# Optimization experiments

Hardware: AMD Instinct MI355X
Metric: run time of the kernel (lower is better)

Reference implementation:

```python
import jax, jax.numpy as jnp
import numpy as np

N = 50000        # nodes
E = 800000       # edges
F_IN = 16        # num_features
F_EDGE = 8       # num_edge_features
H = 4            # heads
C = 32           # hidden_dim (per-head out channels)
D = H * C        # 128, node state width
NUM_CLASSES = 5
NEG_SLOPE = 0.2  # PyG GATConv default leaky_relu slope


def setup_inputs() -> dict:
    key = jax.random.key(0)
    ks = jax.random.split(key, 30)
    def w(k, shape):
        return jax.random.normal(k, shape, dtype=jnp.float32) * 0.05
    return {
        "x": jax.random.normal(ks[0], (N, F_IN), dtype=jnp.float32),
        "edge_index": jax.random.randint(ks[1], (2, E), 0, N),
        "edge_attr": jax.random.normal(ks[2], (E, F_EDGE), dtype=jnp.float32),
        # edge_encoder: Linear(F_EDGE->C), ReLU, Linear(C->H)
        "ee_w1": w(ks[3], (C, F_EDGE)), "ee_b1": jnp.zeros((C,), jnp.float32),
        "ee_w2": w(ks[4], (H, C)),      "ee_b2": jnp.zeros((H,), jnp.float32),
        # input_proj: Linear(F_IN -> D)
        "proj_w": w(ks[5], (D, F_IN)), "proj_b": jnp.zeros((D,), jnp.float32),
        # conv1: GATConv(F_IN, C, heads=H, edge_dim=H, concat=True)
        "c1_lin": w(ks[6], (D, F_IN)),
        "c1_att_src": w(ks[7], (H, C)), "c1_att_dst": w(ks[8], (H, C)),
        "c1_lin_edge": w(ks[9], (D, H)), "c1_att_edge": w(ks[10], (H, C)),
        "c1_bias": jnp.zeros((D,), jnp.float32),
        # conv2: GATConv(D, C, heads=H, edge_dim=H, concat=True)
        "c2_lin": w(ks[11], (D, D)),
        "c2_att_src": w(ks[12], (H, C)), "c2_att_dst": w(ks[13], (H, C)),
        "c2_lin_edge": w(ks[14], (D, H)), "c2_att_edge": w(ks[15], (H, C)),
        "c2_bias": jnp.zeros((D,), jnp.float32),
        # layer norms
        "n1_g": jnp.ones((D,), jnp.float32), "n1_b": jnp.zeros((D,), jnp.float32),
        "n2_g": jnp.ones((D,), jnp.float32), "n2_b": jnp.zeros((D,), jnp.float32),
        # jk_proj: Linear(3D -> D)
        "jk_w": w(ks[16], (D, 3 * D)), "jk_b": jnp.zeros((D,), jnp.float32),
        # classifier: Linear(D -> NUM_CLASSES)
        "cls_w": w(ks[17], (NUM_CLASSES, D)), "cls_b": jnp.zeros((NUM_CLASSES,), jnp.float32),
    }


def _layer_norm(h, g, b, eps=1e-5):
    mu = jnp.mean(h, axis=-1, keepdims=True)
    var = jnp.var(h, axis=-1, keepdims=True)
    return (h - mu) * jax.lax.rsqrt(var + eps) * g + b


def _gat_conv(x, src, dst, e_attr, lin_w, att_src, att_dst, lin_edge_w, att_edge, bias):
    """PyG GATConv (v1) with edge features, concat=True, eval mode (no dropout)."""
    n = x.shape[0]
    xs = (x @ lin_w.T).reshape(n, H, C)                      # [N,H,C]
    a_src = jnp.einsum('nhc,hc->nh', xs, att_src)            # [N,H]
    a_dst = jnp.einsum('nhc,hc->nh', xs, att_dst)            # [N,H]
    ee = (e_attr @ lin_edge_w.T).reshape(-1, H, C)           # [E,H,C]
    a_edge = jnp.einsum('ehc,hc->eh', ee, att_edge)          # [E,H]
    alpha = jax.nn.leaky_relu(a_src[src] + a_dst[dst] + a_edge, NEG_SLOPE)
    # segment softmax over destination neighborhoods
    amax = jax.ops.segment_max(alpha, dst, num_segments=n)
    ex = jnp.exp(alpha - amax[dst])
    denom = jax.ops.segment_sum(ex, dst, num_segments=n)
    alpha = ex / (denom[dst] + 1e-16)                        # [E,H]
    msg = xs[src] * alpha[:, :, None]                        # [E,H,C]
    out = jax.ops.segment_sum(msg, dst, num_segments=n)      # [N,H,C]
    return out.reshape(n, H * C) + bias


def reference(x, edge_index, edge_attr,
              ee_w1, ee_b1, ee_w2, ee_b2,
              proj_w, proj_b,
              c1_lin, c1_att_src, c1_att_dst, c1_lin_edge, c1_att_edge, c1_bias,
              c2_lin, c2_att_src, c2_att_dst, c2_lin_edge, c2_att_edge, c2_bias,
              n1_g, n1_b, n2_g, n2_b,
              jk_w, jk_b, cls_w, cls_b):
    src, dst = edge_index[0], edge_index[1]
    # edge encoder
    e = jax.nn.relu(edge_attr @ ee_w1.T + ee_b1) @ ee_w2.T + ee_b2   # [E,H]
    h0 = x @ proj_w.T + proj_b                                        # [N,D]
    h1 = _gat_conv(x, src, dst, e, c1_lin, c1_att_src, c1_att_dst,
                   c1_lin_edge, c1_att_edge, c1_bias)
    h1 = _layer_norm(jax.nn.elu(h1) + h0, n1_g, n1_b)
    h2 = _gat_conv(h1, src, dst, e, c2_lin, c2_att_src, c2_att_dst,
                   c2_lin_edge, c2_att_edge, c2_bias)
    h2 = _layer_norm(jax.nn.elu(h2) + h1, n2_g, n2_b)
    h = jnp.concatenate([h0, h1, h2], axis=-1) @ jk_w.T + jk_b
    out = h @ cls_w.T + cls_b
    return jax.nn.log_softmax(out, axis=1)
```

## Files before the change

kernel.cpp:

```cpp
#include <hip/hip_runtime.h>
#include <cstdint>

#define NN 50000
#define NE 800000
#define DPX 6250
#define SLICES 391

using short8  = __attribute__((ext_vector_type(8))) short;
using float4v = __attribute__((ext_vector_type(4))) float;

__device__ __forceinline__ ushort f2bf(float f) {
    uint u = __float_as_uint(f);
    uint r = (u + 0x7fffu + ((u >> 16) & 1u)) >> 16;
    return (ushort)r;
}
__device__ __forceinline__ float bf2f(uint u) {
    return __uint_as_float(u << 16);
}

__global__ __launch_bounds__(256) void k_prep2(const float* __restrict__ le1, const float* __restrict__ ae1,
                                               const float* __restrict__ le2, const float* __restrict__ ae2,
                                               const float* __restrict__ jkw, const float* __restrict__ jkb,
                                               const float* __restrict__ clw, const float* __restrict__ clb,
                                               const float* __restrict__ projw, const float* __restrict__ c1lin,
                                               const float* __restrict__ c2lin,
                                               const float* __restrict__ asrc1, const float* __restrict__ adst1,
                                               float* __restrict__ M, float* __restrict__ CW,
                                               float* __restrict__ cbp,
                                               ushort* __restrict__ w01b, ushort* __restrict__ c2b,
                                               float* __restrict__ Vmat, int* __restrict__ deg)
{
    int idx = blockIdx.x * 256 + threadIdx.x;
    if (idx < NN) deg[idx] = 0;
    if (idx < 32) {
        const float* le = (idx < 16) ? le1 : le2;
        const float* ae = (idx < 16) ? ae1 : ae2;
        int hk = idx & 15, h = hk >> 2, k = hk & 3;
        float s = 0.f;
        for (int c = 0; c < 32; ++c)
            s += le[(h * 32 + c) * 4 + k] * ae[h * 32 + c];
        M[idx] = s;
    } else if (idx < 1952) {
        int o = idx - 32;
        int r = o / 384, c = o - r * 384;
        float s = 0.f;
        for (int k = 0; k < 128; ++k)
            s += clw[r * 128 + k] * jkw[(size_t)k * 384 + c];
        CW[o] = s;
    } else if (idx < 1957) {
        int r = idx - 1952;
        float s = clb[r];
        for (int k = 0; k < 128; ++k)
            s += clw[r * 128 + k] * jkb[k];
        cbp[r] = s;
    } else if (idx >= 2048 && idx < 10240) {
        int o = idx - 2048;
        int r = o >> 5, c = o & 31;
        float v = 0.f;
        if (c < 16) v = (r < 128) ? projw[r * 16 + c] : c1lin[(r - 128) * 16 + c];
        w01b[o] = f2bf(v);
    } else if (idx >= 10240 && idx < 26624) {
        int o = idx - 10240;
        c2b[o] = f2bf(c2lin[o]);
    } else if (idx >= 26624 && idx < 26752) {
        int o = idx - 26624;
        const float* att = (o < 64) ? asrc1 : adst1;
        int oo = o & 63, h = oo >> 4, k = oo & 15;
        float s = 0.f;
        for (int c = 0; c < 32; ++c)
            s += c1lin[(h * 32 + c) * 16 + k] * att[h * 32 + c];
        Vmat[o] = s;
    }
}

__global__ __launch_bounds__(256) void k_att1(const float* __restrict__ x,
                                              const float* __restrict__ V,
                                              float* __restrict__ as_o,
                                              float* __restrict__ ad_o)
{
    __shared__ float sV[128];
    int t = threadIdx.x;
    if (t < 128) sV[t] = V[t];
    __syncthreads();
    int n = blockIdx.x * 256 + t;
    if (n >= NN) return;
    const float4* xr = (const float4*)(x + (size_t)n * 16);
    float4 x0 = xr[0], x1 = xr[1], x2 = xr[2], x3 = xr[3];
    float xv[16] = {x0.x,x0.y,x0.z,x0.w, x1.x,x1.y,x1.z,x1.w,
                    x2.x,x2.y,x2.z,x2.w, x3.x,x3.y,x3.z,x3.w};
    float s[4], d[4];
    #pragma unroll
    for (int h = 0; h < 4; ++h) {
        float ss = 0.f, dd = 0.f;
        #pragma unroll
        for (int k = 0; k < 16; ++k) {
            ss += xv[k] * sV[h * 16 + k];
            dd += xv[k] * sV[64 + h * 16 + k];
        }
        s[h] = ss; d[h] = dd;
    }
    *(float4*)(as_o + (size_t)n * 4) = make_float4(s[0], s[1], s[2], s[3]);
    *(float4*)(ad_o + (size_t)n * 4) = make_float4(d[0], d[1], d[2], d[3]);
}

__global__ __launch_bounds__(256) void k_edge_mlp(const float* __restrict__ ea,
                                                  const float* __restrict__ w1,
                                                  const float* __restrict__ b1,
                                                  const float* __restrict__ w2,
                                                  const float* __restrict__ b2,
                                                  const int* __restrict__ ei,
                                                  const float* __restrict__ Mm,
                                                  const float* __restrict__ as1,
                                                  const float* __restrict__ ad1,
                                                  ushort* __restrict__ exb,
                                                  ushort* __restrict__ ae2)
{
    __shared__ float sw1[256], sb1[32], sw2[128], sb2[4], sM[32];
    int t = threadIdx.x;
    sw1[t] = w1[t];
    if (t < 128) sw2[t] = w2[t];
    if (t < 32)  { sb1[t] = b1[t]; sM[t] = Mm[t]; }
    if (t < 4)   sb2[t] = b2[t];
    __syncthreads();
    int e = blockIdx.x * 256 + t;
    if (e >= NE) return;
    int src = ei[e], dst = ei[NE + e];
    float4 s4 = *(const float4*)(as1 + (size_t)src * 4);
    float4 d4 = *(const float4*)(ad1 + (size_t)dst * 4);
    float4 x0 = *(const float4*)(ea + (size_t)e * 8);
    float4 x1 = *(const float4*)(ea + (size_t)e * 8 + 4);
    float o0 = sb2[0], o1 = sb2[1], o2 = sb2[2], o3 = sb2[3];
    #pragma unroll
    for (int j = 0; j < 32; ++j) {
        const float* w = sw1 + j * 8;
        float s = sb1[j] + w[0]*x0.x + w[1]*x0.y + w[2]*x0.z + w[3]*x0.w
                         + w[4]*x1.x + w[5]*x1.y + w[6]*x1.z + w[7]*x1.w;
        s = fmaxf(s, 0.f);
        o0 += sw2[0*32+j] * s; o1 += sw2[1*32+j] * s;
        o2 += sw2[2*32+j] * s; o3 += sw2[3*32+j] * s;
    }
    float sa[4] = {s4.x, s4.y, s4.z, s4.w};
    float da[4] = {d4.x, d4.y, d4.z, d4.w};
    ushort exq[4], a2q[4];
    #pragma unroll
    for (int h = 0; h < 4; ++h) {
        float ae1 = sM[h*4+0]*o0 + sM[h*4+1]*o1 + sM[h*4+2]*o2 + sM[h*4+3]*o3;
        float al = sa[h] + da[h] + ae1;
        al = al > 0.f ? al : 0.2f * al;
        exq[h] = f2bf(__expf(al));
        a2q[h] = f2bf(sM[16+h*4+0]*o0 + sM[16+h*4+1]*o1 + sM[16+h*4+2]*o2 + sM[16+h*4+3]*o3);
    }
    *(uint2*)(exb + (size_t)e * 4) =
        make_uint2((uint)exq[0] | ((uint)exq[1] << 16), (uint)exq[2] | ((uint)exq[3] << 16));
    *(uint2*)(ae2 + (size_t)e * 4) =
        make_uint2((uint)a2q[0] | ((uint)a2q[1] << 16), (uint)a2q[2] | ((uint)a2q[3] << 16));
}

__global__ __launch_bounds__(256) void k_hist8(const int* __restrict__ ei, int* __restrict__ deg)
{
    int grp = blockIdx.x & 7;
    int base = (blockIdx.x >> 3) * 2048 + threadIdx.x;
    #pragma unroll
    for (int k = 0; k < 8; ++k) {
        int e = base + k * 256;
        if (e < NE) {
            int dst = ei[NE + e];
            if (dst / DPX == grp) atomicAdd(&deg[dst], 1);
        }
    }
}

__global__ __launch_bounds__(256) void k_scan_blk(const int* __restrict__ deg,
                                                  int* __restrict__ loc,
                                                  int* __restrict__ bsum)
{
    __shared__ int tmp[256];
    int t = threadIdx.x;
    int i = blockIdx.x * 256 + t;
    int v = (i < NN) ? deg[i] : 0;
    tmp[t] = v;
    __syncthreads();
    #pragma unroll
    for (int o = 1; o < 256; o <<= 1) {
        int add = (t >= o) ? tmp[t - o] : 0;
        __syncthreads();
        tmp[t] += add;
        __syncthreads();
    }
    if (i < NN) loc[i] = tmp[t] - v;
    if (t == 255) bsum[blockIdx.x] = tmp[255];
}

__global__ __launch_bounds__(256) void k_scan_top(const int* __restrict__ bsum,
                                                  int* __restrict__ bcarry,
                                                  int* __restrict__ total_out, int nb)
{
    __shared__ int tmp[256];
    int t = threadIdx.x;
    int v = (t < nb) ? bsum[t] : 0;
    tmp[t] = v;
    __syncthreads();
    #pragma unroll
    for (int o = 1; o < 256; o <<= 1) {
        int add = (t >= o) ? tmp[t - o] : 0;
        __syncthreads();
        tmp[t] += add;
        __syncthreads();
    }
    if (t < nb) bcarry[t] = tmp[t] - v;
    if (t == 255) *total_out = tmp[255];
}

__global__ __launch_bounds__(256) void k_scan_add(const int* __restrict__ loc,
                                                  const int* __restrict__ bcarry,
                                                  int* __restrict__ off,
                                                  int* __restrict__ cur)
{
    int i = blockIdx.x * 256 + threadIdx.x;
    if (i < NN) {
        int o = loc[i] + bcarry[blockIdx.x];
        off[i] = o;
        cur[i] = o;
    }
}

__global__ __launch_bounds__(256) void k_scatter8(const int* __restrict__ ei,
                                                  const ushort* __restrict__ exb,
                                                  int* __restrict__ cursor,
                                                  int4* __restrict__ csr4)
{
    int grp = blockIdx.x & 7;
    int base = (blockIdx.x >> 3) * 2048 + threadIdx.x;
    #pragma unroll
    for (int k = 0; k < 8; ++k) {
        int e = base + k * 256;
        if (e < NE) {
            int dst = ei[NE + e];
            if (dst / DPX == grp) {
                int src = ei[e];
                uint2 ex = *(const uint2*)(exb + (size_t)e * 4);
                int p = atomicAdd(&cursor[dst], 1);
                csr4[p] = make_int4((src << 16) | dst, e, (int)ex.x, (int)ex.y);
            }
        }
    }
}

__global__ __launch_bounds__(256) void k_gemm1(const float* __restrict__ x,
                                               const ushort* __restrict__ w01,
                                               const float* __restrict__ pbias,
                                               ushort* __restrict__ hcatb,
                                               ushort* __restrict__ xs, int M)
{
    int t = threadIdx.x;
    int wv = t >> 6, lane = t & 63;
    int quad = lane >> 4, r16 = lane & 15;
    int m0 = blockIdx.x * 128 + wv * 32;
    int ar0 = m0 + r16;      if (ar0 >= M) ar0 = M - 1;
    int ar1 = m0 + 16 + r16; if (ar1 >= M) ar1 = M - 1;
    short8 a0 = (short8){0,0,0,0,0,0,0,0}, a1 = a0;
    if (quad < 2) {
        const float* p0 = x + (size_t)ar0 * 16 + quad * 8;
        const float* p1 = x + (size_t)ar1 * 16 + quad * 8;
        float4 u0 = *(const float4*)p0, u1 = *(const float4*)(p0 + 4);
        float4 v0 = *(const float4*)p1, v1 = *(const float4*)(p1 + 4);
        a0[0]=(short)f2bf(u0.x); a0[1]=(short)f2bf(u0.y); a0[2]=(short)f2bf(u0.z); a0[3]=(short)f2bf(u0.w);
        a0[4]=(short)f2bf(u1.x); a0[5]=(short)f2bf(u1.y); a0[6]=(short)f2bf(u1.z); a0[7]=(short)f2bf(u1.w);
        a1[0]=(short)f2bf(v0.x); a1[1]=(short)f2bf(v0.y); a1[2]=(short)f2bf(v0.z); a1[3]=(short)f2bf(v0.w);
        a1[4]=(short)f2bf(v1.x); a1[5]=(short)f2bf(v1.y); a1[6]=(short)f2bf(v1.z); a1[7]=(short)f2bf(v1.w);
    }
    float4v acc[2][16];
    #pragma unroll
    for (int i = 0; i < 2; ++i)
        #pragma unroll
        for (int j = 0; j < 16; ++j) acc[i][j] = (float4v){0.f, 0.f, 0.f, 0.f};
    #pragma unroll
    for (int nt = 0; nt < 16; ++nt) {
        short8 b = *(const short8*)(w01 + (size_t)(nt * 16 + r16) * 32 + quad * 8);
        acc[0][nt] = __builtin_amdgcn_mfma_f32_16x16x32_bf16(a0, b, acc[0][nt], 0, 0, 0);
        acc[1][nt] = __builtin_amdgcn_mfma_f32_16x16x32_bf16(a1, b, acc[1][nt], 0, 0, 0);
    }
    #pragma unroll
    for (int rt = 0; rt < 2; ++rt) {
        #pragma unroll
        for (int nt = 0; nt < 16; ++nt) {
            int col = (nt & 7) * 16 + r16;
            float bv = (nt < 8) ? pbias[col] : 0.f;
            #pragma unroll
            for (int r = 0; r < 4; ++r) {
                int row = m0 + rt * 16 + quad * 4 + r;
                if (row < M) {
                    float v = acc[rt][nt][r] + bv;
                    if (nt < 8) hcatb[(size_t)row * 384 + col] = f2bf(v);
                    else        xs[(size_t)row * 128 + col] = f2bf(v);
                }
            }
        }
    }
}

__global__ __launch_bounds__(256) void k_gemm2(const ushort* __restrict__ A,
                                               const ushort* __restrict__ W,
                                               const float* __restrict__ atts,
                                               const float* __restrict__ attd,
                                               ushort* __restrict__ xs,
                                               float* __restrict__ as_o,
                                               float* __restrict__ ad_o, int M)
{
    __shared__ float sAs[128], sAd[128];
    int t = threadIdx.x;
    if (t < 128) { sAs[t] = atts[t]; sAd[t] = attd[t]; }
    __syncthreads();
    int wv = t >> 6, lane = t & 63;
    int quad = lane >> 4, r16 = lane & 15;
    int m0 = blockIdx.x * 128 + wv * 32;
    float4v acc[2][8];
    #pragma unroll
    for (int i = 0; i < 2; ++i)
        #pragma unroll
        for (int j = 0; j < 8; ++j) acc[i][j] = (float4v){0.f, 0.f, 0.f, 0.f};
    int ar0 = m0 + r16;      if (ar0 >= M) ar0 = M - 1;
    int ar1 = m0 + 16 + r16; if (ar1 >= M) ar1 = M - 1;
    const ushort* a0p = A + (size_t)ar0 * 384 + quad * 8;
    const ushort* a1p = A + (size_t)ar1 * 384 + quad * 8;
    const ushort* wp  = W + (size_t)r16 * 128 + quad * 8;
    #pragma unroll
    for (int k0 = 0; k0 < 128; k0 += 32) {
        short8 a0 = *(const short8*)(a0p + k0);
        short8 a1 = *(const short8*)(a1p + k0);
        #pragma unroll
        for (int nt = 0; nt < 8; ++nt) {
            short8 b = *(const short8*)(wp + (size_t)(nt * 16) * 128 + k0);
            acc[0][nt] = __builtin_amdgcn_mfma_f32_16x16x32_bf16(a0, b, acc[0][nt], 0, 0, 0);
            acc[1][nt] = __builtin_amdgcn_mfma_f32_16x16x32_bf16(a1, b, acc[1][nt], 0, 0, 0);
        }
    }
    #pragma unroll
    for (int rt = 0; rt < 2; ++rt) {
        #pragma unroll
        for (int nt = 0; nt < 8; ++nt) {
            int col = nt * 16 + r16;
            #pragma unroll
            for (int r = 0; r < 4; ++r) {
                int row = m0 + rt * 16 + quad * 4 + r;
                if (row < M)
                    xs[(size_t)row * 128 + col] = f2bf(acc[rt][nt][r]);
            }
        }
        #pragma unroll
        for (int r = 0; r < 4; ++r) {
            int row = m0 + rt * 16 + quad * 4 + r;
            float sh[4], dh[4];
            #pragma unroll
            for (int h = 0; h < 4; ++h) {
                int cA = h * 32 + r16, cB = cA + 16;
                sh[h] = acc[rt][2*h][r] * sAs[cA] + acc[rt][2*h+1][r] * sAs[cB];
                dh[h] = acc[rt][2*h][r] * sAd[cA] + acc[rt][2*h+1][r] * sAd[cB];
            }
            #pragma unroll
            for (int o = 1; o < 16; o <<= 1) {
                #pragma unroll
                for (int h = 0; h < 4; ++h) {
                    sh[h] += __shfl_xor(sh[h], o, 64);
                    dh[h] += __shfl_xor(dh[h], o, 64);
                }
            }
            if (r16 == 0 && row < M) {
                *(float4*)(as_o + (size_t)row * 4) = make_float4(sh[0], sh[1], sh[2], sh[3]);
                *(float4*)(ad_o + (size_t)row * 4) = make_float4(dh[0], dh[1], dh[2], dh[3]);
            }
        }
    }
}

__global__ __launch_bounds__(256) void k_soft2csr(int4* __restrict__ csr4,
                                                  const float* __restrict__ as_in,
                                                  const float* __restrict__ ad_in,
                                                  const ushort* __restrict__ ae2)
{
    int i = blockIdx.x * 256 + threadIdx.x;
    if (i >= NE) return;
    int4 en = csr4[i];
    uint sd = (uint)en.x;
    int src = (int)(sd >> 16), dst = (int)(sd & 0xffffu);
    float4 s4 = *(const float4*)(as_in + (size_t)src * 4);
    float4 d4 = *(const float4*)(ad_in + (size_t)dst * 4);
    uint2 aq = *(const uint2*)(ae2 + (size_t)en.y * 4);
    float av[4] = {bf2f(aq.x & 0xffffu), bf2f(aq.x >> 16), bf2f(aq.y & 0xffffu), bf2f(aq.y >> 16)};
    float sa[4] = {s4.x, s4.y, s4.z, s4.w};
    float da[4] = {d4.x, d4.y, d4.z, d4.w};
    ushort exq[4];
    #pragma unroll
    for (int h = 0; h < 4; ++h) {
        float al = sa[h] + da[h] + av[h];
        al = al > 0.f ? al : 0.2f * al;
        exq[h] = f2bf(__expf(al));
    }
    en.z = (int)((uint)exq[0] | ((uint)exq[1] << 16));
    en.w = (int)((uint)exq[2] | ((uint)exq[3] << 16));
    csr4[i] = en;
}

__global__ __launch_bounds__(256) void k_agg2(const int* __restrict__ off,
                                              const int4* __restrict__ csr4,
                                              const ushort* __restrict__ xs,
                                              const float* __restrict__ bias,
                                              const ushort* __restrict__ residb,
                                              const float* __restrict__ g,
                                              const float* __restrict__ bln,
                                              ushort* __restrict__ outb)
{
    int wave = threadIdx.x >> 6;
    int lane = threadIdx.x & 63;
    int n = blockIdx.x * 4 + wave;
    if (n >= NN) return;
    int i0 = off[n], i1 = off[n + 1];
    int c0 = lane * 2;
    int h = lane >> 4;
    int hsel = h >> 1, hsh = (h & 1) << 4;
    float a0 = 0.f, a1 = 0.f, den = 0.f;
    int i = i0;
    for (; i + 8 <= i1; i += 8) {
        int4 en[8];
        #pragma unroll
        for (int j = 0; j < 8; ++j) en[j] = csr4[i + j];
        uint p[8];
        #pragma unroll
        for (int j = 0; j < 8; ++j)
            p[j] = *(const uint*)(xs + (size_t)((uint)en[j].x >> 16) * 128 + c0);
        #pragma unroll
        for (int j = 0; j < 8; ++j) {
            uint exsel = (uint)(hsel ? en[j].w : en[j].z);
            float w = bf2f((exsel >> hsh) & 0xffffu);
            a0 = fmaf(bf2f(p[j] & 0xffffu), w, a0);
            a1 = fmaf(bf2f(p[j] >> 16), w, a1);
            den += w;
        }
    }
    for (; i + 4 <= i1; i += 4) {
        int4 en[4];
        #pragma unroll
        for (int j = 0; j < 4; ++j) en[j] = csr4[i + j];
        uint p[4];
        #pragma unroll
        for (int j = 0; j < 4; ++j)
            p[j] = *(const uint*)(xs + (size_t)((uint)en[j].x >> 16) * 128 + c0);
        #pragma unroll
        for (int j = 0; j < 4; ++j) {
            uint exsel = (uint)(hsel ? en[j].w : en[j].z);
            float w = bf2f((exsel >> hsh) & 0xffffu);
            a0 = fmaf(bf2f(p[j] & 0xffffu), w, a0);
            a1 = fmaf(bf2f(p[j] >> 16), w, a1);
            den += w;
        }
    }
    for (; i < i1; ++i) {
        int4 en = csr4[i];
        uint p0 = *(const uint*)(xs + (size_t)((uint)en.x >> 16) * 128 + c0);
        uint exsel = (uint)(hsel ? en.w : en.z);
        float w = bf2f((exsel >> hsh) & 0xffffu);
        a0 = fmaf(bf2f(p0 & 0xffffu), w, a0);
        a1 = fmaf(bf2f(p0 >> 16), w, a1);
        den += w;
    }
    float inv = 1.f / (den + 1e-16f);
    float v0 = a0 * inv + bias[c0];
    float v1 = a1 * inv + bias[c0 + 1];
    v0 = v0 > 0.f ? v0 : (__expf(v0) - 1.f);
    v1 = v1 > 0.f ? v1 : (__expf(v1) - 1.f);
    uint rp = *(const uint*)(residb + (size_t)n * 384 + c0);
    float r0 = v0 + bf2f(rp & 0xffffu);
    float r1 = v1 + bf2f(rp >> 16);
    float ssum = r0 + r1, ssq = r0 * r0 + r1 * r1;
    #pragma unroll
    for (int o = 1; o < 64; o <<= 1) {
        ssum += __shfl_xor(ssum, o, 64);
        ssq  += __shfl_xor(ssq, o, 64);
    }
    float mu = ssum * (1.f / 128.f);
    float var = ssq * (1.f / 128.f) - mu * mu;
    float rs = rsqrtf(var + 1e-5f);
    float o0 = (r0 - mu) * rs * g[c0] + bln[c0];
    float o1 = (r1 - mu) * rs * g[c0 + 1] + bln[c0 + 1];
    uint pk = (uint)f2bf(o0) | ((uint)f2bf(o1) << 16);
    *(uint*)(outb + (size_t)n * 384 + c0) = pk;
}

__global__ __launch_bounds__(256) void k_cls(const ushort* __restrict__ hcatb,
                                             const float* __restrict__ CW,
                                             const float* __restrict__ cbp,
                                             float* __restrict__ out)
{
    __shared__ float sCW[1920], scb[5];
    int t = threadIdx.x;
    for (int i = t; i < 1920; i += 256) sCW[i] = CW[i];
    if (t < 5) scb[t] = cbp[t];
    __syncthreads();
    int n = blockIdx.x * 256 + t;
    if (n >= NN) return;
    float acc[5] = {scb[0], scb[1], scb[2], scb[3], scb[4]};
    const uint2* hr = (const uint2*)(hcatb + (size_t)n * 384);
    #pragma unroll 4
    for (int q = 0; q < 96; ++q) {
        uint2 p = hr[q];
        float v0 = bf2f(p.x & 0xffffu), v1 = bf2f(p.x >> 16);
        float v2 = bf2f(p.y & 0xffffu), v3 = bf2f(p.y >> 16);
        #pragma unroll
        for (int o = 0; o < 5; ++o) {
            const float* w = sCW + o * 384 + q * 4;
            acc[o] += v0*w[0] + v1*w[1] + v2*w[2] + v3*w[3];
        }
    }
    float m = acc[0];
    #pragma unroll
    for (int o = 1; o < 5; ++o) m = fmaxf(m, acc[o]);
    float sum = 0.f;
    #pragma unroll
    for (int o = 0; o < 5; ++o) sum += __expf(acc[o] - m);
    float lse = __logf(sum) + m;
    float* op = out + (size_t)n * 5;
    #pragma unroll
    for (int o = 0; o < 5; ++o) op[o] = acc[o] - lse;
}

extern "C" void kernel_launch(void* const* d_in, const int* in_sizes, int n_in,
                              void* d_out, int out_size, void* d_ws, size_t ws_size,
                              hipStream_t stream)
{
    (void)in_sizes; (void)n_in; (void)out_size; (void)ws_size;
    const float* x        = (const float*)d_in[0];
    const int*   ei       = (const int*)d_in[1];
    const float* eattr    = (const float*)d_in[2];
    const float* ee_w1    = (const float*)d_in[3];
    const float* ee_b1    = (const float*)d_in[4];
    const float* ee_w2    = (const float*)d_in[5];
    const float* ee_b2    = (const float*)d_in[6];
    const float* proj_w   = (const float*)d_in[7];
    const float* proj_b   = (const float*)d_in[8];
    const float* c1_lin   = (const float*)d_in[9];
    const float* c1_asrc  = (const float*)d_in[10];
    const float* c1_adst  = (const float*)d_in[11];
    const float* c1_ledge = (const float*)d_in[12];
    const float* c1_aedge = (const float*)d_in[13];
    const float* c1_bias  = (const float*)d_in[14];
    const float* c2_lin   = (const float*)d_in[15];
    const float* c2_asrc  = (const float*)d_in[16];
    const float* c2_adst  = (const float*)d_in[17];
    const float* c2_ledge = (const float*)d_in[18];
    const float* c2_aedge = (const float*)d_in[19];
    const float* c2_bias  = (const float*)d_in[20];
    const float* n1_g     = (const float*)d_in[21];
    const float* n1_b     = (const float*)d_in[22];
    const float* n2_g     = (const float*)d_in[23];
    const float* n2_b     = (const float*)d_in[24];
    const float* jk_w     = (const float*)d_in[25];
    const float* jk_b     = (const float*)d_in[26];
    const float* cls_w    = (const float*)d_in[27];
    const float* cls_b    = (const float*)d_in[28];
    float* out = (float*)d_out;
    float* ws  = (float*)d_ws;

    const size_t oM   = 0;
    const size_t oCW  = 64;
    const size_t oCB  = 1984;
    const size_t oV   = 2048;
    const size_t oEX  = 2176;
    const size_t oAE2 = oEX + (size_t)NE * 2;
    const size_t oHB  = oAE2 + (size_t)NE * 2;
    const size_t oXS  = oHB + (size_t)NN * 192;
    const size_t oWB  = oXS + (size_t)NN * 64;
    const size_t oAS  = oWB + 12288;
    const size_t oAD  = oAS + (size_t)NN * 4;
    const size_t oI   = oAD + (size_t)NN * 4;

    float*  Mmat  = ws + oM;
    float*  CW    = ws + oCW;
    float*  cbp   = ws + oCB;
    float*  Vmat  = ws + oV;
    ushort* exb   = (ushort*)(ws + oEX);
    ushort* ae2b  = (ushort*)(ws + oAE2);
    ushort* hcatb = (ushort*)(ws + oHB);
    ushort* xs    = (ushort*)(ws + oXS);
    ushort* w01b  = (ushort*)(ws + oWB);
    ushort* c2b   = w01b + 8192;
    float*  as_b  = ws + oAS;
    float*  ad_b  = ws + oAD;
    int*    ip    = (int*)(ws + oI);
    int*    deg   = ip;
    int*    loc   = ip + NN;
    int*    off   = ip + 2 * NN;
    int*    cur   = ip + 3 * NN + 16;
    int*    bsum  = ip + 4 * NN + 16;
    int*    bcar  = ip + 4 * NN + 272;
    int4*   csr4  = (int4*)(ip + 4 * NN + 544);

    const int EB  = (NE + 255) / 256;
    const int NB  = (NN + 255) / 256;
    const int GB  = (NN + 127) / 128;
    const int WB2 = (NN + 3) / 4;
    const int PB  = SLICES * 8;

    k_prep2<<<NB, 256, 0, stream>>>(c1_ledge, c1_aedge, c2_ledge, c2_aedge,
                                    jk_w, jk_b, cls_w, cls_b,
                                    proj_w, c1_lin, c2_lin, c1_asrc, c1_adst,
                                    Mmat, CW, cbp, w01b, c2b, Vmat, deg);
    k_att1<<<NB, 256, 0, stream>>>(x, Vmat, as_b, ad_b);
    k_edge_mlp<<<EB, 256, 0, stream>>>(eattr, ee_w1, ee_b1, ee_w2, ee_b2, ei,
                                       Mmat, as_b, ad_b, exb, ae2b);
    k_hist8<<<PB, 256, 0, stream>>>(ei, deg);
    k_scan_blk<<<NB, 256, 0, stream>>>(deg, loc, bsum);
    k_scan_top<<<1, 256, 0, stream>>>(bsum, bcar, off + NN, NB);
    k_scan_add<<<NB, 256, 0, stream>>>(loc, bcar, off, cur);
    k_scatter8<<<PB, 256, 0, stream>>>(ei, exb, cur, csr4);

    k_gemm1<<<GB, 256, 0, stream>>>(x, w01b, proj_b, hcatb, xs, NN);

    k_agg2<<<WB2, 256, 0, stream>>>(off, csr4, xs, c1_bias, hcatb,
                                    n1_g, n1_b, hcatb + 128);

    k_gemm2<<<GB, 256, 0, stream>>>(hcatb + 128, c2b, c2_asrc, c2_adst,
                                    xs, as_b, ad_b, NN);
    k_soft2csr<<<EB, 256, 0, stream>>>(csr4, as_b, ad_b, ae2b);
    k_agg2<<<WB2, 256, 0, stream>>>(off, csr4, xs, c2_bias, hcatb + 128,
                                    n2_g, n2_b, hcatb + 256);

    k_cls<<<NB, 256, 0, stream>>>(hcatb, CW, cbp, out);
}
```

Measured before the change: 393.4 us.

## Store gathered node features as FP8 and pre-permute edge attention into CSR order

The projected node features that the aggregation kernels gather per edge are now stored as FP8 (e4m3) instead of bf16. This halves the bytes of the random gather traffic in both aggregation passes, and the values are converted back with the packed fp8-to-f32 instruction. Separately, the second-layer edge attention terms are written in CSR order during the scatter, so the softmax kernel reads them sequentially instead of through the original edge index. The softmax kernel also now writes only the half of the CSR entry that changes. FP8 storage reduces precision of the message values and may affect accuracy.

```diff
diff --git a/kernel.cpp b/kernel.cpp
--- a/kernel.cpp
+++ b/kernel.cpp
@@ -8,6 +8,8 @@
 
 using short8  = __attribute__((ext_vector_type(8))) short;
 using float4v = __attribute__((ext_vector_type(4))) float;
+using floatx2 = __attribute__((ext_vector_type(2))) float;
+typedef unsigned char uchar;
 
 __device__ __forceinline__ ushort f2bf(float f) {
     uint u = __float_as_uint(f);
@@ -16,6 +18,9 @@
 }
 __device__ __forceinline__ float bf2f(uint u) {
     return __uint_as_float(u << 16);
+}
+__device__ __forceinline__ uchar f2fp8(float v) {
+    return (uchar)((uint)__builtin_amdgcn_cvt_pk_fp8_f32(v, v, 0, false) & 0xffu);
 }
 
 __global__ __launch_bounds__(256) void k_prep2(const float* __restrict__ le1, const float* __restrict__ ae1,
@@ -226,8 +231,10 @@
 
 __global__ __launch_bounds__(256) void k_scatter8(const int* __restrict__ ei,
                                                   const ushort* __restrict__ exb,
+                                                  const ushort* __restrict__ ae2b,
                                                   int* __restrict__ cursor,
-                                                  int4* __restrict__ csr4)
+                                                  int4* __restrict__ csr4,
+                                                  uint2* __restrict__ ae2csr)
 {
     int grp = blockIdx.x & 7;
     int base = (blockIdx.x >> 3) * 2048 + threadIdx.x;
@@ -239,8 +246,10 @@
             if (dst / DPX == grp) {
                 int src = ei[e];
                 uint2 ex = *(const uint2*)(exb + (size_t)e * 4);
+                uint2 ae = *(const uint2*)(ae2b + (size_t)e * 4);
                 int p = atomicAdd(&cursor[dst], 1);
                 csr4[p] = make_int4((src << 16) | dst, e, (int)ex.x, (int)ex.y);
+                ae2csr[p] = ae;
             }
         }
     }
@@ -250,7 +259,7 @@
                                                const ushort* __restrict__ w01,
                                                const float* __restrict__ pbias,
                                                ushort* __restrict__ hcatb,
-                                               ushort* __restrict__ xs, int M)
+                                               uchar* __restrict__ xs8, int M)
 {
     int t = threadIdx.x;
     int wv = t >> 6, lane = t & 63;
@@ -292,7 +301,7 @@
                 if (row < M) {
                     float v = acc[rt][nt][r] + bv;
                     if (nt < 8) hcatb[(size_t)row * 384 + col] = f2bf(v);
-                    else        xs[(size_t)row * 128 + col] = f2bf(v);
+                    else        xs8[(size_t)row * 128 + col] = f2fp8(v);
                 }
             }
         }
@@ -303,7 +312,7 @@
                                                const ushort* __restrict__ W,
                                                const float* __restrict__ atts,
                                                const float* __restrict__ attd,
-                                               ushort* __restrict__ xs,
+                                               uchar* __restrict__ xs8,
                                                float* __restrict__ as_o,
                                                float* __restrict__ ad_o, int M)
 {
@@ -344,7 +353,7 @@
             for (int r = 0; r < 4; ++r) {
                 int row = m0 + rt * 16 + quad * 4 + r;
                 if (row < M)
-                    xs[(size_t)row * 128 + col] = f2bf(acc[rt][nt][r]);
+                    xs8[(size_t)row * 128 + col] = f2fp8(acc[rt][nt][r]);
             }
         }
         #pragma unroll
@@ -374,18 +383,17 @@
 }
 
 __global__ __launch_bounds__(256) void k_soft2csr(int4* __restrict__ csr4,
+                                                  const uint2* __restrict__ ae2csr,
                                                   const float* __restrict__ as_in,
-                                                  const float* __restrict__ ad_in,
-                                                  const ushort* __restrict__ ae2)
+                                                  const float* __restrict__ ad_in)
 {
     int i = blockIdx.x * 256 + threadIdx.x;
     if (i >= NE) return;
-    int4 en = csr4[i];
-    uint sd = (uint)en.x;
+    uint sd = (uint)csr4[i].x;
     int src = (int)(sd >> 16), dst = (int)(sd & 0xffffu);
     float4 s4 = *(const float4*)(as_in + (size_t)src * 4);
     float4 d4 = *(const float4*)(ad_in + (size_t)dst * 4);
-    uint2 aq = *(const uint2*)(ae2 + (size_t)en.y * 4);
+    uint2 aq = ae2csr[i];
     float av[4] = {bf2f(aq.x & 0xffffu), bf2f(aq.x >> 16), bf2f(aq.y & 0xffffu), bf2f(aq.y >> 16)};
     float sa[4] = {s4.x, s4.y, s4.z, s4.w};
     float da[4] = {d4.x, d4.y, d4.z, d4.w};
@@ -396,14 +404,13 @@
         al = al > 0.f ? al : 0.2f * al;
         exq[h] = f2bf(__expf(al));
     }
-    en.z = (int)((uint)exq[0] | ((uint)exq[1] << 16));
-    en.w = (int)((uint)exq[2] | ((uint)exq[3] << 16));
-    csr4[i] = en;
+    ((uint2*)&csr4[i])[1] =
+        make_uint2((uint)exq[0] | ((uint)exq[1] << 16), (uint)exq[2] | ((uint)exq[3] << 16));
 }
 
 __global__ __launch_bounds__(256) void k_agg2(const int* __restrict__ off,
                                               const int4* __restrict__ csr4,
-                                              const ushort* __restrict__ xs,
+                                              const uchar* __restrict__ xs8,
                                               const float* __restrict__ bias,
                                               const ushort* __restrict__ residb,
                                               const float* __restrict__ g,
@@ -424,16 +431,17 @@
         int4 en[8];
         #pragma unroll
         for (int j = 0; j < 8; ++j) en[j] = csr4[i + j];
-        uint p[8];
+        ushort p[8];
         #pragma unroll
         for (int j = 0; j < 8; ++j)
-            p[j] = *(const uint*)(xs + (size_t)((uint)en[j].x >> 16) * 128 + c0);
+            p[j] = *(const ushort*)(xs8 + (size_t)((uint)en[j].x >> 16) * 128 + c0);
         #pragma unroll
         for (int j = 0; j < 8; ++j) {
             uint exsel = (uint)(hsel ? en[j].w : en[j].z);
             float w = bf2f((exsel >> hsh) & 0xffffu);
-            a0 = fmaf(bf2f(p[j] & 0xffffu), w, a0);
-            a1 = fmaf(bf2f(p[j] >> 16), w, a1);
+            floatx2 v = __builtin_amdgcn_cvt_pk_f32_fp8((int)(uint)p[j], false);
+            a0 = fmaf(v.x, w, a0);
+            a1 = fmaf(v.y, w, a1);
             den += w;
         }
     }
@@ -441,26 +449,28 @@
         int4 en[4];
         #pragma unroll
         for (int j = 0; j < 4; ++j) en[j] = csr4[i + j];
-        uint p[4];
+        ushort p[4];
         #pragma unroll
         for (int j = 0; j < 4; ++j)
-            p[j] = *(const uint*)(xs + (size_t)((uint)en[j].x >> 16) * 128 + c0);
+            p[j] = *(const ushort*)(xs8 + (size_t)((uint)en[j].x >> 16) * 128 + c0);
         #pragma unroll
         for (int j = 0; j < 4; ++j) {
             uint exsel = (uint)(hsel ? en[j].w : en[j].z);
             float w = bf2f((exsel >> hsh) & 0xffffu);
-            a0 = fmaf(bf2f(p[j] & 0xffffu), w, a0);
-            a1 = fmaf(bf2f(p[j] >> 16), w, a1);
+            floatx2 v = __builtin_amdgcn_cvt_pk_f32_fp8((int)(uint)p[j], false);
+            a0 = fmaf(v.x, w, a0);
+            a1 = fmaf(v.y, w, a1);
             den += w;
         }
     }
     for (; i < i1; ++i) {
         int4 en = csr4[i];
-        uint p0 = *(const uint*)(xs + (size_t)((uint)en.x >> 16) * 128 + c0);
+        ushort p0 = *(const ushort*)(xs8 + (size_t)((uint)en.x >> 16) * 128 + c0);
         uint exsel = (uint)(hsel ? en.w : en.z);
         float w = bf2f((exsel >> hsh) & 0xffffu);
-        a0 = fmaf(bf2f(p0 & 0xffffu), w, a0);
-        a1 = fmaf(bf2f(p0 >> 16), w, a1);
+        floatx2 v = __builtin_amdgcn_cvt_pk_f32_fp8((int)(uint)p0, false);
+        a0 = fmaf(v.x, w, a0);
+        a1 = fmaf(v.y, w, a1);
         den += w;
     }
     float inv = 1.f / (den + 1e-16f);
@@ -568,7 +578,7 @@
     const size_t oAE2 = oEX + (size_t)NE * 2;
     const size_t oHB  = oAE2 + (size_t)NE * 2;
     const size_t oXS  = oHB + (size_t)NN * 192;
-    const size_t oWB  = oXS + (size_t)NN * 64;
+    const size_t oWB  = oXS + (size_t)NN * 32;
     const size_t oAS  = oWB + 12288;
     const size_t oAD  = oAS + (size_t)NN * 4;
     const size_t oI   = oAD + (size_t)NN * 4;
@@ -580,19 +590,20 @@
     ushort* exb   = (ushort*)(ws + oEX);
     ushort* ae2b  = (ushort*)(ws + oAE2);
     ushort* hcatb = (ushort*)(ws + oHB);
-    ushort* xs    = (ushort*)(ws + oXS);
+    uchar*  xs8   = (uchar*)(ws + oXS);
     ushort* w01b  = (ushort*)(ws + oWB);
     ushort* c2b   = w01b + 8192;
     float*  as_b  = ws + oAS;
     float*  ad_b  = ws + oAD;
     int*    ip    = (int*)(ws + oI);
-    int*    deg   = ip;
-    int*    loc   = ip + NN;
-    int*    off   = ip + 2 * NN;
-    int*    cur   = ip + 3 * NN + 16;
-    int*    bsum  = ip + 4 * NN + 16;
-    int*    bcar  = ip + 4 * NN + 272;
-    int4*   csr4  = (int4*)(ip + 4 * NN + 544);
+    int*    deg    = ip;
+    int*    loc    = ip + NN;
+    int*    off    = ip + 2 * NN;
+    int*    cur    = ip + 3 * NN + 16;
+    int*    bsum   = ip + 4 * NN + 16;
+    int*    bcar   = ip + 4 * NN + 272;
+    int4*   csr4   = (int4*)(ip + 4 * NN + 544);
+    uint2*  ae2csr = (uint2*)(ip + 4 * NN + 544 + 4 * (size_t)NE);
 
     const int EB  = (NE + 255) / 256;
     const int NB  = (NN + 255) / 256;
@@ -611,17 +622,17 @@
     k_scan_blk<<<NB, 256, 0, stream>>>(deg, loc, bsum);
     k_scan_top<<<1, 256, 0, stream>>>(bsum, bcar, off + NN, NB);
     k_scan_add<<<NB, 256, 0, stream>>>(loc, bcar, off, cur);
-    k_scatter8<<<PB, 256, 0, stream>>>(ei, exb, cur, csr4);
-
-    k_gemm1<<<GB, 256, 0, stream>>>(x, w01b, proj_b, hcatb, xs, NN);
-
-    k_agg2<<<WB2, 256, 0, stream>>>(off, csr4, xs, c1_bias, hcatb,
+    k_scatter8<<<PB, 256, 0, stream>>>(ei, exb, ae2b, cur, csr4, ae2csr);
+
+    k_gemm1<<<GB, 256, 0, stream>>>(x, w01b, proj_b, hcatb, xs8, NN);
+
+    k_agg2<<<WB2, 256, 0, stream>>>(off, csr4, xs8, c1_bias, hcatb,
                                     n1_g, n1_b, hcatb + 128);
 
     k_gemm2<<<GB, 256, 0, stream>>>(hcatb + 128, c2b, c2_asrc, c2_adst,
-                                    xs, as_b, ad_b, NN);
-    k_soft2csr<<<EB, 256, 0, stream>>>(csr4, as_b, ad_b, ae2b);
-    k_agg2<<<WB2, 256, 0, stream>>>(off, csr4, xs, c2_bias, hcatb + 128,
+                                    xs8, as_b, ad_b, NN);
+    k_soft2csr<<<EB, 256, 0, stream>>>(csr4, ae2csr, as_b, ad_b);
+    k_agg2<<<WB2, 256, 0, stream>>>(off, csr4, xs8, c2_bias, hcatb + 128,
                                     n2_g, n2_b, hcatb + 256);
 
     k_cls<<<NB, 256, 0, stream>>>(hcatb, CW, cbp, out);
```

New measurement: 393.5 us. Within noise of the previous version (+0.0%).

## Store node features as head-major fp8 and split aggregation per head

Applied to the files above, without the earlier changes.

Node features xs are now stored in fp8 in a head-major layout [head][node][32], so each gather fetches 32 bytes per head instead of 256-byte bf16 rows. The per-edge layer-2 edge attention terms are packed as fp8 directly into the CSR entries, which removes a separate indexed load in k_soft2csr. The fused aggregation kernel is split into k_aggH, which handles one head per block group across half of the nodes, and k_epi, which does normalization, ELU, residual and LayerNorm. This trades extra intermediate traffic and fp8 precision loss on activations for smaller gather footprints with better cache locality.

```diff
diff --git a/kernel.cpp b/kernel.cpp
--- a/kernel.cpp
+++ b/kernel.cpp
@@ -8,6 +8,8 @@
 
 using short8  = __attribute__((ext_vector_type(8))) short;
 using float4v = __attribute__((ext_vector_type(4))) float;
+using floatx2 = __attribute__((ext_vector_type(2))) float;
+typedef unsigned char uchar;
 
 __device__ __forceinline__ ushort f2bf(float f) {
     uint u = __float_as_uint(f);
@@ -16,6 +18,13 @@
 }
 __device__ __forceinline__ float bf2f(uint u) {
     return __uint_as_float(u << 16);
+}
+__device__ __forceinline__ uchar f2fp8(float v) {
+    return (uchar)((uint)__builtin_amdgcn_cvt_pk_fp8_f32(v, v, 0, false) & 0xffu);
+}
+__device__ __forceinline__ float fp8f(uint b) {
+    floatx2 v = __builtin_amdgcn_cvt_pk_f32_fp8((int)b, false);
+    return v.x;
 }
 
 __global__ __launch_bounds__(256) void k_prep2(const float* __restrict__ le1, const float* __restrict__ ae1,
@@ -113,7 +122,7 @@
                                                   const float* __restrict__ as1,
                                                   const float* __restrict__ ad1,
                                                   ushort* __restrict__ exb,
-                                                  ushort* __restrict__ ae2)
+                                                  uint* __restrict__ aeq)
 {
     __shared__ float sw1[256], sb1[32], sw2[128], sb2[4], sM[32];
     int t = threadIdx.x;
@@ -141,19 +150,21 @@
     }
     float sa[4] = {s4.x, s4.y, s4.z, s4.w};
     float da[4] = {d4.x, d4.y, d4.z, d4.w};
-    ushort exq[4], a2q[4];
+    ushort exq[4];
+    float a2[4];
     #pragma unroll
     for (int h = 0; h < 4; ++h) {
         float ae1 = sM[h*4+0]*o0 + sM[h*4+1]*o1 + sM[h*4+2]*o2 + sM[h*4+3]*o3;
         float al = sa[h] + da[h] + ae1;
         al = al > 0.f ? al : 0.2f * al;
         exq[h] = f2bf(__expf(al));
-        a2q[h] = f2bf(sM[16+h*4+0]*o0 + sM[16+h*4+1]*o1 + sM[16+h*4+2]*o2 + sM[16+h*4+3]*o3);
+        a2[h] = sM[16+h*4+0]*o0 + sM[16+h*4+1]*o1 + sM[16+h*4+2]*o2 + sM[16+h*4+3]*o3;
     }
     *(uint2*)(exb + (size_t)e * 4) =
         make_uint2((uint)exq[0] | ((uint)exq[1] << 16), (uint)exq[2] | ((uint)exq[3] << 16));
-    *(uint2*)(ae2 + (size_t)e * 4) =
-        make_uint2((uint)a2q[0] | ((uint)a2q[1] << 16), (uint)a2q[2] | ((uint)a2q[3] << 16));
+    uint q = (uint)__builtin_amdgcn_cvt_pk_fp8_f32(a2[0], a2[1], 0, false);
+    q = (uint)__builtin_amdgcn_cvt_pk_fp8_f32(a2[2], a2[3], (int)q, true);
+    aeq[e] = q;
 }
 
 __global__ __launch_bounds__(256) void k_hist8(const int* __restrict__ ei, int* __restrict__ deg)
@@ -226,6 +237,7 @@
 
 __global__ __launch_bounds__(256) void k_scatter8(const int* __restrict__ ei,
                                                   const ushort* __restrict__ exb,
+                                                  const uint* __restrict__ aeq,
                                                   int* __restrict__ cursor,
                                                   int4* __restrict__ csr4)
 {
@@ -239,8 +251,9 @@
             if (dst / DPX == grp) {
                 int src = ei[e];
                 uint2 ex = *(const uint2*)(exb + (size_t)e * 4);
+                uint q = aeq[e];
                 int p = atomicAdd(&cursor[dst], 1);
-                csr4[p] = make_int4((src << 16) | dst, e, (int)ex.x, (int)ex.y);
+                csr4[p] = make_int4((src << 16) | dst, (int)ex.x, (int)ex.y, (int)q);
             }
         }
     }
@@ -250,7 +263,7 @@
                                                const ushort* __restrict__ w01,
                                                const float* __restrict__ pbias,
                                                ushort* __restrict__ hcatb,
-                                               ushort* __restrict__ xs, int M)
+                                               uchar* __restrict__ xs8h, int M)
 {
     int t = threadIdx.x;
     int wv = t >> 6, lane = t & 63;
@@ -292,7 +305,7 @@
                 if (row < M) {
                     float v = acc[rt][nt][r] + bv;
                     if (nt < 8) hcatb[(size_t)row * 384 + col] = f2bf(v);
-                    else        xs[(size_t)row * 128 + col] = f2bf(v);
+                    else        xs8h[((size_t)(col >> 5) * NN + row) * 32 + (col & 31)] = f2fp8(v);
                 }
             }
         }
@@ -303,7 +316,7 @@
                                                const ushort* __restrict__ W,
                                                const float* __restrict__ atts,
                                                const float* __restrict__ attd,
-                                               ushort* __restrict__ xs,
+                                               uchar* __restrict__ xs8h,
                                                float* __restrict__ as_o,
                                                float* __restrict__ ad_o, int M)
 {
@@ -344,7 +357,7 @@
             for (int r = 0; r < 4; ++r) {
                 int row = m0 + rt * 16 + quad * 4 + r;
                 if (row < M)
-                    xs[(size_t)row * 128 + col] = f2bf(acc[rt][nt][r]);
+                    xs8h[((size_t)(col >> 5) * NN + row) * 32 + (col & 31)] = f2fp8(acc[rt][nt][r]);
             }
         }
         #pragma unroll
@@ -375,8 +388,7 @@
 
 __global__ __launch_bounds__(256) void k_soft2csr(int4* __restrict__ csr4,
                                                   const float* __restrict__ as_in,
-                                                  const float* __restrict__ ad_in,
-                                                  const ushort* __restrict__ ae2)
+                                                  const float* __restrict__ ad_in)
 {
     int i = blockIdx.x * 256 + threadIdx.x;
     if (i >= NE) return;
@@ -385,8 +397,9 @@
     int src = (int)(sd >> 16), dst = (int)(sd & 0xffffu);
     float4 s4 = *(const float4*)(as_in + (size_t)src * 4);
     float4 d4 = *(const float4*)(ad_in + (size_t)dst * 4);
-    uint2 aq = *(const uint2*)(ae2 + (size_t)en.y * 4);
-    float av[4] = {bf2f(aq.x & 0xffffu), bf2f(aq.x >> 16), bf2f(aq.y & 0xffffu), bf2f(aq.y >> 16)};
+    floatx2 a01 = __builtin_amdgcn_cvt_pk_f32_fp8(en.w, false);
+    floatx2 a23 = __builtin_amdgcn_cvt_pk_f32_fp8(en.w, true);
+    float av[4] = {a01.x, a01.y, a23.x, a23.y};
     float sa[4] = {s4.x, s4.y, s4.z, s4.w};
     float da[4] = {d4.x, d4.y, d4.z, d4.w};
     ushort exq[4];
@@ -396,94 +409,94 @@
         al = al > 0.f ? al : 0.2f * al;
         exq[h] = f2bf(__expf(al));
     }
-    en.z = (int)((uint)exq[0] | ((uint)exq[1] << 16));
-    en.w = (int)((uint)exq[2] | ((uint)exq[3] << 16));
+    en.y = (int)((uint)exq[0] | ((uint)exq[1] << 16));
+    en.z = (int)((uint)exq[2] | ((uint)exq[3] << 16));
     csr4[i] = en;
 }
 
-__global__ __launch_bounds__(256) void k_agg2(const int* __restrict__ off,
+__global__ __launch_bounds__(256) void k_aggH(const int* __restrict__ off,
                                               const int4* __restrict__ csr4,
-                                              const ushort* __restrict__ xs,
-                                              const float* __restrict__ bias,
-                                              const ushort* __restrict__ residb,
-                                              const float* __restrict__ g,
-                                              const float* __restrict__ bln,
-                                              ushort* __restrict__ outb)
-{
-    int wave = threadIdx.x >> 6;
-    int lane = threadIdx.x & 63;
-    int n = blockIdx.x * 4 + wave;
+                                              const uchar* __restrict__ xs8h,
+                                              ushort* __restrict__ aggH,
+                                              float* __restrict__ denH)
+{
+    int g = blockIdx.x & 7;
+    int head = g >> 1;
+    int bi = blockIdx.x >> 3;
+    int wave = threadIdx.x >> 6, lane = threadIdx.x & 63;
+    int n = (g & 1) * (NN / 2) + bi * 4 + wave;
     if (n >= NN) return;
     int i0 = off[n], i1 = off[n + 1];
-    int c0 = lane * 2;
-    int h = lane >> 4;
-    int hsel = h >> 1, hsh = (h & 1) << 4;
-    float a0 = 0.f, a1 = 0.f, den = 0.f;
-    int i = i0;
-    for (; i + 8 <= i1; i += 8) {
-        int4 en[8];
-        #pragma unroll
-        for (int j = 0; j < 8; ++j) en[j] = csr4[i + j];
-        uint p[8];
-        #pragma unroll
-        for (int j = 0; j < 8; ++j)
-            p[j] = *(const uint*)(xs + (size_t)((uint)en[j].x >> 16) * 128 + c0);
-        #pragma unroll
-        for (int j = 0; j < 8; ++j) {
-            uint exsel = (uint)(hsel ? en[j].w : en[j].z);
-            float w = bf2f((exsel >> hsh) & 0xffffu);
-            a0 = fmaf(bf2f(p[j] & 0xffffu), w, a0);
-            a1 = fmaf(bf2f(p[j] >> 16), w, a1);
-            den += w;
-        }
-    }
-    for (; i + 4 <= i1; i += 4) {
-        int4 en[4];
-        #pragma unroll
-        for (int j = 0; j < 4; ++j) en[j] = csr4[i + j];
-        uint p[4];
-        #pragma unroll
-        for (int j = 0; j < 4; ++j)
-            p[j] = *(const uint*)(xs + (size_t)((uint)en[j].x >> 16) * 128 + c0);
-        #pragma unroll
-        for (int j = 0; j < 4; ++j) {
-            uint exsel = (uint)(hsel ? en[j].w : en[j].z);
-            float w = bf2f((exsel >> hsh) & 0xffffu);
-            a0 = fmaf(bf2f(p[j] & 0xffffu), w, a0);
-            a1 = fmaf(bf2f(p[j] >> 16), w, a1);
-            den += w;
-        }
-    }
-    for (; i < i1; ++i) {
-        int4 en = csr4[i];
-        uint p0 = *(const uint*)(xs + (size_t)((uint)en.x >> 16) * 128 + c0);
-        uint exsel = (uint)(hsel ? en.w : en.z);
-        float w = bf2f((exsel >> hsh) & 0xffffu);
-        a0 = fmaf(bf2f(p0 & 0xffffu), w, a0);
-        a1 = fmaf(bf2f(p0 >> 16), w, a1);
-        den += w;
-    }
-    float inv = 1.f / (den + 1e-16f);
-    float v0 = a0 * inv + bias[c0];
-    float v1 = a1 * inv + bias[c0 + 1];
-    v0 = v0 > 0.f ? v0 : (__expf(v0) - 1.f);
-    v1 = v1 > 0.f ? v1 : (__expf(v1) - 1.f);
-    uint rp = *(const uint*)(residb + (size_t)n * 384 + c0);
-    float r0 = v0 + bf2f(rp & 0xffffu);
-    float r1 = v1 + bf2f(rp >> 16);
-    float ssum = r0 + r1, ssq = r0 * r0 + r1 * r1;
-    #pragma unroll
-    for (int o = 1; o < 64; o <<= 1) {
-        ssum += __shfl_xor(ssum, o, 64);
-        ssq  += __shfl_xor(ssq, o, 64);
-    }
-    float mu = ssum * (1.f / 128.f);
-    float var = ssq * (1.f / 128.f) - mu * mu;
+    int j = lane >> 5, c = lane & 31;
+    int hsel = head >> 1, hsh = (head & 1) << 4;
+    const uchar* xt = xs8h + (size_t)head * NN * 32 + c;
+    float a = 0.f, den = 0.f;
+    int i = i0 + j;
+    for (; i + 6 < i1; i += 8) {
+        int4 e0 = csr4[i], e1 = csr4[i+2], e2 = csr4[i+4], e3 = csr4[i+6];
+        uint b0 = xt[(size_t)((uint)e0.x >> 16) * 32];
+        uint b1 = xt[(size_t)((uint)e1.x >> 16) * 32];
+        uint b2 = xt[(size_t)((uint)e2.x >> 16) * 32];
+        uint b3 = xt[(size_t)((uint)e3.x >> 16) * 32];
+        float w0 = bf2f(((uint)(hsel ? e0.z : e0.y) >> hsh) & 0xffffu);
+        float w1 = bf2f(((uint)(hsel ? e1.z : e1.y) >> hsh) & 0xffffu);
+        float w2 = bf2f(((uint)(hsel ? e2.z : e2.y) >> hsh) & 0xffffu);
+        float w3 = bf2f(((uint)(hsel ? e3.z : e3.y) >> hsh) & 0xffffu);
+        a = fmaf(fp8f(b0), w0, a); a = fmaf(fp8f(b1), w1, a);
+        a = fmaf(fp8f(b2), w2, a); a = fmaf(fp8f(b3), w3, a);
+        den += (w0 + w1) + (w2 + w3);
+    }
+    for (; i < i1; i += 2) {
+        int4 e0 = csr4[i];
+        uint b0 = xt[(size_t)((uint)e0.x >> 16) * 32];
+        float w0 = bf2f(((uint)(hsel ? e0.z : e0.y) >> hsh) & 0xffffu);
+        a = fmaf(fp8f(b0), w0, a);
+        den += w0;
+    }
+    a += __shfl_xor(a, 32, 64);
+    den += __shfl_xor(den, 32, 64);
+    if (lane < 32) aggH[((size_t)head * NN + n) * 32 + c] = f2bf(a);
+    if (lane == 0) denH[(size_t)head * NN + n] = den;
+}
+
+__global__ __launch_bounds__(256) void k_epi(const ushort* __restrict__ aggH,
+                                             const float* __restrict__ denH,
+                                             const float* __restrict__ bias,
+                                             const ushort* __restrict__ residb,
+                                             const float* __restrict__ g,
+                                             const float* __restrict__ bln,
+                                             ushort* __restrict__ outb)
+{
+    __shared__ float red[4][2];
+    int t = threadIdx.x;
+    int n = blockIdx.x * 2 + (t >> 7);
+    int c = t & 127;
+    float r = 0.f;
+    if (n < NN) {
+        int h = c >> 5, cc = c & 31;
+        float a = bf2f(aggH[((size_t)h * NN + n) * 32 + cc]);
+        float den = denH[(size_t)h * NN + n];
+        float v = a / (den + 1e-16f) + bias[c];
+        v = v > 0.f ? v : (__expf(v) - 1.f);
+        r = v + bf2f(residb[(size_t)n * 384 + c]);
+    }
+    float s = r, sq = r * r;
+    #pragma unroll
+    for (int o = 32; o > 0; o >>= 1) {
+        s  += __shfl_down(s, o, 64);
+        sq += __shfl_down(sq, o, 64);
+    }
+    int wave = t >> 6;
+    if ((t & 63) == 0) { red[wave][0] = s; red[wave][1] = sq; }
+    __syncthreads();
+    int base = (t >> 7) * 2;
+    float S  = red[base][0] + red[base + 1][0];
+    float SQ = red[base][1] + red[base + 1][1];
+    float mu = S * (1.f / 128.f);
+    float var = SQ * (1.f / 128.f) - mu * mu;
     float rs = rsqrtf(var + 1e-5f);
-    float o0 = (r0 - mu) * rs * g[c0] + bln[c0];
-    float o1 = (r1 - mu) * rs * g[c0 + 1] + bln[c0 + 1];
-    uint pk = (uint)f2bf(o0) | ((uint)f2bf(o1) << 16);
-    *(uint*)(outb + (size_t)n * 384 + c0) = pk;
+    if (n < NN)
+        outb[(size_t)n * 384 + c] = f2bf((r - mu) * rs * g[c] + bln[c]);
 }
 
 __global__ __launch_bounds__(256) void k_cls(const ushort* __restrict__ hcatb,
@@ -565,10 +578,12 @@
     const size_t oCB  = 1984;
     const size_t oV   = 2048;
     const size_t oEX  = 2176;
-    const size_t oAE2 = oEX + (size_t)NE * 2;
-    const size_t oHB  = oAE2 + (size_t)NE * 2;
+    const size_t oAQ  = oEX + (size_t)NE * 2;
+    const size_t oHB  = oAQ + (size_t)NE;
     const size_t oXS  = oHB + (size_t)NN * 192;
-    const size_t oWB  = oXS + (size_t)NN * 64;
+    const size_t oAG  = oXS + (size_t)NN * 32;
+    const size_t oDN  = oAG + (size_t)NN * 64;
+    const size_t oWB  = oDN + (size_t)NN * 4;
     const size_t oAS  = oWB + 12288;
     const size_t oAD  = oAS + (size_t)NN * 4;
     const size_t oI   = oAD + (size_t)NN * 4;
@@ -578,9 +593,11 @@
     float*  cbp   = ws + oCB;
     float*  Vmat  = ws + oV;
     ushort* exb   = (ushort*)(ws + oEX);
-    ushort* ae2b  = (ushort*)(ws + oAE2);
+    uint*   aeq   = (uint*)(ws + oAQ);
     ushort* hcatb = (ushort*)(ws + oHB);
-    ushort* xs    = (ushort*)(ws + oXS);
+    uchar*  xs8h  = (uchar*)(ws + oXS);
+    ushort* aggH  = (ushort*)(ws + oAG);
+    float*  denH  = ws + oDN;
     ushort* w01b  = (ushort*)(ws + oWB);
     ushort* c2b   = w01b + 8192;
     float*  as_b  = ws + oAS;
@@ -597,8 +614,9 @@
     const int EB  = (NE + 255) / 256;
     const int NB  = (NN + 255) / 256;
     const int GB  = (NN + 127) / 128;
-    const int WB2 = (NN + 3) / 4;
     const int PB  = SLICES * 8;
+    const int AB  = (NN / 2 / 4) * 8;
+    const int PEB = NN / 2;
 
     k_prep2<<<NB, 256, 0, stream>>>(c1_ledge, c1_aedge, c2_ledge, c2_aedge,
                                     jk_w, jk_b, cls_w, cls_b,
@@ -606,23 +624,23 @@
                                     Mmat, CW, cbp, w01b, c2b, Vmat, deg);
     k_att1<<<NB, 256, 0, stream>>>(x, Vmat, as_b, ad_b);
     k_edge_mlp<<<EB, 256, 0, stream>>>(eattr, ee_w1, ee_b1, ee_w2, ee_b2, ei,
-                                       Mmat, as_b, ad_b, exb, ae2b);
+                                       Mmat, as_b, ad_b, exb, aeq);
     k_hist8<<<PB, 256, 0, stream>>>(ei, deg);
     k_scan_blk<<<NB, 256, 0, stream>>>(deg, loc, bsum);
     k_scan_top<<<1, 256, 0, stream>>>(bsum, bcar, off + NN, NB);
     k_scan_add<<<NB, 256, 0, stream>>>(loc, bcar, off, cur);
-    k_scatter8<<<PB, 256, 0, stream>>>(ei, exb, cur, csr4);
-
-    k_gemm1<<<GB, 256, 0, stream>>>(x, w01b, proj_b, hcatb, xs, NN);
-
-    k_agg2<<<WB2, 256, 0, stream>>>(off, csr4, xs, c1_bias, hcatb,
-                                    n1_g, n1_b, hcatb + 128);
+    k_scatter8<<<PB, 256, 0, stream>>>(ei, exb, aeq, cur, csr4);
+
+    k_gemm1<<<GB, 256, 0, stream>>>(x, w01b, proj_b, hcatb, xs8h, NN);
+
+    k_aggH<<<AB, 256, 0, stream>>>(off, csr4, xs8h, aggH, denH);
+    k_epi<<<PEB, 256, 0, stream>>>(aggH, denH, c1_bias, hcatb, n1_g, n1_b, hcatb + 128);
 
     k_gemm2<<<GB, 256, 0, stream>>>(hcatb + 128, c2b, c2_asrc, c2_adst,
-                                    xs, as_b, ad_b, NN);
-    k_soft2csr<<<EB, 256, 0, stream>>>(csr4, as_b, ad_b, ae2b);
-    k_agg2<<<WB2, 256, 0, stream>>>(off, csr4, xs, c2_bias, hcatb + 128,
-                                    n2_g, n2_b, hcatb + 256);
+                                    xs8h, as_b, ad_b, NN);
+    k_soft2csr<<<EB, 256, 0, stream>>>(csr4, as_b, ad_b);
+    k_aggH<<<AB, 256, 0, stream>>>(off, csr4, xs8h, aggH, denH);
+    k_epi<<<PEB, 256, 0, stream>>>(aggH, denH, c2_bias, hcatb + 128, n2_g, n2_b, hcatb + 256);
 
     k_cls<<<NB, 256, 0, stream>>>(hcatb, CW, cbp, out);
 }
```

Result: slower. 510.4 us (+29.7%).
